# Kernel optimization log

Hardware: AMD Instinct MI355X
Metric: run time of the kernel (lower is better)

## Reference

```python
import jax, jax.numpy as jnp
import numpy as np

B, C_IN, C_OUT, F, K = 4, 64, 64, 50000, 16
BN_EPS = 1e-5


def setup_inputs() -> dict:
    key = jax.random.key(0)
    k1, k2, k3, k4 = jax.random.split(key, 4)
    fea = jax.random.normal(k1, (B, C_IN, F), dtype=jnp.float32)
    ring_n = jax.random.randint(k2, (B, F, K), 0, F, dtype=jnp.int64)
    # Conv1d(kernel_size=1) weight [out, in] and bias [out]
    W = jax.random.normal(k3, (C_OUT, C_IN), dtype=jnp.float32) / np.sqrt(C_IN)
    b = jax.random.normal(k4, (C_OUT,), dtype=jnp.float32) * 0.01
    gamma = jnp.ones((C_OUT,), dtype=jnp.float32)
    beta = jnp.zeros((C_OUT,), dtype=jnp.float32)
    return {"fea": fea, "ring_n": ring_n, "W": W, "b": b, "gamma": gamma, "beta": beta}


def reference(fea, ring_n, W, b, gamma, beta):
    # Note: original torch code overwrites the cat result, so only the
    # NEIGHBOR features are summed (center face excluded).
    def gather_sum(f, r):  # f: [C, F], r: [F, K]
        return f[:, r].sum(axis=-1)  # [C, F, K] -> [C, F]

    summed = jax.vmap(gather_sum)(fea, ring_n)  # [B, C_in, F]
    # 1x1 conv == channel matmul
    y = jnp.einsum("oc,bcf->bof", W, summed) + b[None, :, None]  # [B, C_out, F]
    # BatchNorm1d (training mode): stats over (batch, faces) per channel
    mean = y.mean(axis=(0, 2), keepdims=True)
    var = y.var(axis=(0, 2), keepdims=True)  # biased, as torch BN uses for normalization
    y = (y - mean) * jax.lax.rsqrt(var + BN_EPS)
    y = y * gamma[None, :, None] + beta[None, :, None]
    return jax.nn.relu(y)
```

## Files before the change

kernel.cpp:

```cpp
#include <hip/hip_runtime.h>
#include <hip/hip_bf16.h>
#include <stdint.h>

#define Bn 4
#define Cn 64
#define Fn 50000
#define Kn 16
#define NTOT (Bn*Fn)
#define EPS 1e-5f

typedef unsigned short u16;
typedef unsigned int u32;
typedef __attribute__((ext_vector_type(8))) short short8;
typedef __attribute__((ext_vector_type(4))) float f32x4;
typedef __attribute__((ext_vector_type(4))) int i32x4;
typedef __attribute__((ext_vector_type(4))) unsigned int u32x4;

__device__ __forceinline__ u16 f2bf(float x) {
  __hip_bfloat16 h = __float2bfloat16(x);
  return *reinterpret_cast<u16*>(&h);
}
__device__ __forceinline__ u32 pack2(float a, float b) {
  return (u32)f2bf(a) | ((u32)f2bf(b) << 16);
}

__global__ __launch_bounds__(256) void k1_mfma(
    const float* __restrict__ fea, const float* __restrict__ W,
    u32* __restrict__ Gt) {
  const int b = blockIdx.y;
  const int f0 = blockIdx.x * 128;
  const int t = threadIdx.x;
  const int l = t & 63;
  const int quad = l >> 4;
  const int lane15 = l & 15;
  const int wv = t >> 6;
  __shared__ float a_s[64][129];

  short8 afr[4][2];
  #pragma unroll
  for (int ot = 0; ot < 4; ot++) {
    #pragma unroll
    for (int kk = 0; kk < 2; kk++) {
      const float* wr = W + (ot * 16 + lane15) * 64 + kk * 32 + quad * 8;
      float4 wa = *(const float4*)wr;
      float4 wb = *(const float4*)(wr + 4);
      union { short8 v; u32 u[4]; } fr;
      fr.u[0] = pack2(wa.x, wa.y); fr.u[1] = pack2(wa.z, wa.w);
      fr.u[2] = pack2(wb.x, wb.y); fr.u[3] = pack2(wb.z, wb.w);
      afr[ot][kk] = fr.v;
    }
  }

  {
    const float* fb = fea + (size_t)b * Cn * Fn;
    const int f4 = t & 31;
    const int cbase = t >> 5;
    const bool fvalid = (f0 + f4 * 4) < Fn;
    #pragma unroll
    for (int jj = 0; jj < 8; jj++) {
      int c = cbase + jj * 8;
      float4 v = make_float4(0.f, 0.f, 0.f, 0.f);
      if (fvalid) v = *(const float4*)(fb + (size_t)c * Fn + f0 + f4 * 4);
      *(float4*)&a_s[c][f4 * 4] = v;
    }
  }
  __syncthreads();

  f32x4 acc[4][2];
  #pragma unroll
  for (int ot = 0; ot < 4; ot++)
    #pragma unroll
    for (int ft = 0; ft < 2; ft++) acc[ot][ft] = (f32x4){0.f, 0.f, 0.f, 0.f};

  #pragma unroll
  for (int ft = 0; ft < 2; ft++) {
    const int fl = wv * 32 + ft * 16 + lane15;
    float x[16];
    #pragma unroll
    for (int j = 0; j < 8; j++) x[j] = a_s[quad * 8 + j][fl];
    #pragma unroll
    for (int j = 0; j < 8; j++) x[8 + j] = a_s[32 + quad * 8 + j][fl];
    union { short8 s; u32 u[4]; } b0, b1;
    #pragma unroll
    for (int p = 0; p < 4; p++) {
      b0.u[p] = pack2(x[2 * p], x[2 * p + 1]);
      b1.u[p] = pack2(x[8 + 2 * p], x[8 + 2 * p + 1]);
    }
    #pragma unroll
    for (int ot = 0; ot < 4; ot++) {
      acc[ot][ft] = __builtin_amdgcn_mfma_f32_16x16x32_bf16(afr[ot][0], b0.s, acc[ot][ft], 0, 0, 0);
      acc[ot][ft] = __builtin_amdgcn_mfma_f32_16x16x32_bf16(afr[ot][1], b1.s, acc[ot][ft], 0, 0, 0);
    }
  }

  __syncthreads();
  u32* ts = (u32*)&a_s[0][0];
  #pragma unroll
  for (int ot = 0; ot < 4; ot++) {
    #pragma unroll
    for (int ft = 0; ft < 2; ft++) {
      int fl = wv * 32 + ft * 16 + lane15;
      uint2 pv;
      pv.x = pack2(acc[ot][ft][0], acc[ot][ft][1]);
      pv.y = pack2(acc[ot][ft][2], acc[ot][ft][3]);
      *(uint2*)&ts[fl * 36 + ot * 8 + quad * 2] = pv;
    }
  }
  __syncthreads();
  #pragma unroll
  for (int j = 0; j < 4; j++) {
    int o = j * 1024 + t * 4;
    int fl = o >> 5, sl = o & 31;
    if (f0 + fl < Fn) {
      u32x4 vv = *(const u32x4*)&ts[fl * 36 + sl];
      *(u32x4*)(Gt + ((size_t)b * Fn + f0 + fl) * 32 + sl) = vv;
    }
  }
}

template<int WRITE_BF16>
__global__ __launch_bounds__(256) void k2_gather(
    const u32* __restrict__ Gt, const int* __restrict__ ring,
    const float* __restrict__ bias, u32* __restrict__ Y, float* __restrict__ outF,
    float* __restrict__ gsum, float* __restrict__ gsum2) {
  const int bid = blockIdx.x;
  const int b = (bid & 7) >> 1;
  const int sub = ((bid >> 3) << 1) | (bid & 1);
  const int t = threadIdx.x;
  const int gid = t >> 3;
  const int cs = t & 7;

  __shared__ float rs[32][68];
  __shared__ float rs2[32][68];

  float bv[8];
  #pragma unroll
  for (int i = 0; i < 8; i++) bv[i] = bias[cs * 8 + i];

  const u32* Gb = Gt + (size_t)b * Fn * 32;
  const int* rb = ring + (size_t)b * Fn * Kn;

  float sacc[8], s2acc[8];
  #pragma unroll
  for (int i = 0; i < 8; i++) { sacc[i] = 0.f; s2acc[i] = 0.f; }

  const int ntiles = (Fn + 31) / 32;

  int tile = sub;
  i32x4 r0, r1, r2, r3;
  if (tile < ntiles) {
    int fa = tile * 32 + gid;
    int fc = fa < Fn ? fa : Fn - 1;
    const i32x4* rp = (const i32x4*)(rb + (size_t)fc * Kn);
    r0 = __builtin_nontemporal_load(&rp[0]);
    r1 = __builtin_nontemporal_load(&rp[1]);
    r2 = __builtin_nontemporal_load(&rp[2]);
    r3 = __builtin_nontemporal_load(&rp[3]);
  }

  for (; tile < ntiles; tile += 512) {
    const int fa = tile * 32 + gid;
    const bool valid = fa < Fn;
    int idx[16] = {r0[0],r0[1],r0[2],r0[3], r1[0],r1[1],r1[2],r1[3],
                   r2[0],r2[1],r2[2],r2[3], r3[0],r3[1],r3[2],r3[3]};

    const int ntile = tile + 512;
    if (ntile < ntiles) {
      int nfa = ntile * 32 + gid;
      int nfc = nfa < Fn ? nfa : Fn - 1;
      const i32x4* rp = (const i32x4*)(rb + (size_t)nfc * Kn);
      r0 = __builtin_nontemporal_load(&rp[0]);
      r1 = __builtin_nontemporal_load(&rp[1]);
      r2 = __builtin_nontemporal_load(&rp[2]);
      r3 = __builtin_nontemporal_load(&rp[3]);
    }

    float acc[8];
    #pragma unroll
    for (int i = 0; i < 8; i++) acc[i] = 0.f;

    u32x4 v[8];
    #pragma unroll
    for (int k = 0; k < 8; k++)
      v[k] = *(const u32x4*)(Gb + (size_t)idx[k] * 32 + cs * 4);
    #pragma unroll
    for (int k = 0; k < 8; k++) {
      #pragma unroll
      for (int p = 0; p < 4; p++) {
        u32 uu = v[k][p];
        acc[2*p]   += __uint_as_float(uu << 16);
        acc[2*p+1] += __uint_as_float(uu & 0xffff0000u);
      }
    }
    #pragma unroll
    for (int k = 0; k < 8; k++)
      v[k] = *(const u32x4*)(Gb + (size_t)idx[8 + k] * 32 + cs * 4);
    #pragma unroll
    for (int k = 0; k < 8; k++) {
      #pragma unroll
      for (int p = 0; p < 4; p++) {
        u32 uu = v[k][p];
        acc[2*p]   += __uint_as_float(uu << 16);
        acc[2*p+1] += __uint_as_float(uu & 0xffff0000u);
      }
    }

    float yv[8];
    #pragma unroll
    for (int i = 0; i < 8; i++) yv[i] = acc[i] + bv[i];

    if (valid) {
      if (WRITE_BF16) {
        u32x4 pv;
        pv[0] = pack2(yv[0], yv[1]); pv[1] = pack2(yv[2], yv[3]);
        pv[2] = pack2(yv[4], yv[5]); pv[3] = pack2(yv[6], yv[7]);
        __builtin_nontemporal_store(pv,
            (u32x4*)(Y + ((size_t)b * Fn + fa) * 32 + cs * 4));
      } else {
        #pragma unroll
        for (int i = 0; i < 8; i++)
          outF[((size_t)b * 64 + cs * 8 + i) * Fn + fa] = yv[i];
      }
      #pragma unroll
      for (int i = 0; i < 8; i++) {
        sacc[i] += yv[i];
        s2acc[i] += yv[i] * yv[i];
      }
    }
  }

  #pragma unroll
  for (int i = 0; i < 8; i++) {
    rs[gid][cs * 8 + i] = sacc[i];
    rs2[gid][cs * 8 + i] = s2acc[i];
  }
  __syncthreads();
  if (t < 64) {
    float s = 0.f;
    #pragma unroll
    for (int g = 0; g < 32; g++) s += rs[g][t];
    atomicAdd(&gsum[t], s);
  } else if (t < 128) {
    const int ch = t - 64;
    float s2 = 0.f;
    #pragma unroll
    for (int g = 0; g < 32; g++) s2 += rs2[g][ch];
    atomicAdd(&gsum2[ch], s2);
  }
}

__global__ void k3_stats(const float* __restrict__ gsum, const float* __restrict__ gsum2,
                         const float* __restrict__ gamma, const float* __restrict__ beta,
                         float* __restrict__ ab) {
  int o = threadIdx.x;
  if (o < 64) {
    float inv = 1.0f / (float)NTOT;
    float mean = gsum[o] * inv;
    float var = gsum2[o] * inv - mean * mean;
    float r = rsqrtf(var + EPS);
    float a = gamma[o] * r;
    ab[o] = a;
    ab[64 + o] = beta[o] - mean * a;
  }
}

__global__ __launch_bounds__(256) void k4_norm_bf(
    const u32* __restrict__ Y, const float* __restrict__ gsum,
    const float* __restrict__ gsum2, const float* __restrict__ gamma,
    const float* __restrict__ beta, float* __restrict__ out) {
  const int b = blockIdx.y;
  const int f0 = blockIdx.x * 64;
  const int t = threadIdx.x;
  __shared__ u32 ys[32][65];

  #pragma unroll
  for (int j = 0; j < 2; j++) {
    int o = j * 1024 + t * 4;
    int fl = o >> 5, sl = o & 31;
    u32x4 vv = (u32x4)(0u);
    if (f0 + fl < Fn)
      vv = *(const u32x4*)(Y + ((size_t)b * Fn + f0 + fl) * 32 + sl);
    ys[sl + 0][fl] = vv[0]; ys[sl + 1][fl] = vv[1];
    ys[sl + 2][fl] = vv[2]; ys[sl + 3][fl] = vv[3];
  }
  __syncthreads();

  const float inv = 1.0f / (float)NTOT;
  const int fi = t & 15, g = t >> 4;
  const int fbase = 4 * fi;
  #pragma unroll
  for (int j = 0; j < 4; j++) {
    int ch = g * 4 + j;
    float mean = gsum[ch] * inv;
    float var = gsum2[ch] * inv - mean * mean;
    float a = gamma[ch] * rsqrtf(var + EPS);
    float cc = beta[ch] - mean * a;
    if (f0 + fbase < Fn) {
      const int c2 = ch >> 1;
      const bool hi = ch & 1;
      float r[4];
      #pragma unroll
      for (int rr = 0; rr < 4; rr++) {
        u32 u = ys[c2][fbase + rr];
        float xv = __uint_as_float(hi ? (u & 0xffff0000u) : (u << 16));
        r[rr] = fmaxf(fmaf(xv, a, cc), 0.f);
      }
      float4 res = make_float4(r[0], r[1], r[2], r[3]);
      *(float4*)(out + ((size_t)b * 64 + ch) * Fn + f0 + fbase) = res;
    }
  }
}

__global__ __launch_bounds__(256) void k4_norm_f32(float* __restrict__ out,
                                                   const float* __restrict__ ab) {
  int i = blockIdx.x * 256 + threadIdx.x;
  int o = (i / (Fn / 4)) & 63;
  float a = ab[o], c = ab[64 + o];
  float4 v = ((float4*)out)[i];
  v.x = fmaxf(fmaf(v.x, a, c), 0.f);
  v.y = fmaxf(fmaf(v.y, a, c), 0.f);
  v.z = fmaxf(fmaf(v.z, a, c), 0.f);
  v.w = fmaxf(fmaf(v.w, a, c), 0.f);
  ((float4*)out)[i] = v;
}

extern "C" void kernel_launch(void* const* d_in, const int* in_sizes, int n_in,
                              void* d_out, int out_size, void* d_ws, size_t ws_size,
                              hipStream_t stream) {
  const float* fea   = (const float*)d_in[0];
  const int*   ring  = (const int*)d_in[1];
  const float* W     = (const float*)d_in[2];
  const float* bias  = (const float*)d_in[3];
  const float* gamma = (const float*)d_in[4];
  const float* beta  = (const float*)d_in[5];
  float* out = (float*)d_out;

  u32* Gt = (u32*)d_ws;
  const size_t gtBytes = (size_t)Bn * Fn * 32 * 4;
  const size_t yBytes  = (size_t)Bn * Fn * 32 * 4;
  const bool bf16y = ws_size >= gtBytes + yBytes + 1024;

  u32* Y = Gt + (size_t)Bn * Fn * 32;
  float* gsum  = bf16y ? (float*)((char*)d_ws + gtBytes + yBytes)
                       : (float*)((char*)d_ws + gtBytes);
  float* gsum2 = gsum + 64;
  float* ab    = gsum + 128;

  hipMemsetAsync(gsum, 0, 2 * 64 * sizeof(float), stream);
  k1_mfma<<<dim3((Fn + 127) / 128, Bn), 256, 0, stream>>>(fea, W, Gt);
  if (bf16y) {
    k2_gather<1><<<dim3(2048), 256, 0, stream>>>(Gt, ring, bias, Y, out, gsum, gsum2);
    k4_norm_bf<<<dim3((Fn + 63) / 64, Bn), 256, 0, stream>>>(Y, gsum, gsum2, gamma, beta, out);
  } else {
    k2_gather<0><<<dim3(2048), 256, 0, stream>>>(Gt, ring, bias, Y, out, gsum, gsum2);
    k3_stats<<<1, 64, 0, stream>>>(gsum, gsum2, gamma, beta, ab);
    k4_norm_f32<<<dim3((Bn * Cn * Fn / 4) / 256), 256, 0, stream>>>(out, ab);
  }
}
```

Measured before the change: 202.5 us.

## Fuse gather, stats and normalization into one cooperative persistent kernel

Replaces the separate gather and normalize kernels with a single cooperative kernel. It gathers neighbor sums, accumulates the batch-norm statistics, performs a grid-wide sync, then normalizes the bf16 intermediate through a shared-memory transpose. The memset is folded into the first kernel. This removes a launch and a memset, at the cost of a grid barrier and fewer resident blocks in the gather phase, with a fallback to the old path if the cooperative launch fails.

```diff
diff --git a/kernel.cpp b/kernel.cpp
--- a/kernel.cpp
+++ b/kernel.cpp
@@ -1,6 +1,9 @@
 #include <hip/hip_runtime.h>
 #include <hip/hip_bf16.h>
+#include <hip/hip_cooperative_groups.h>
 #include <stdint.h>
+
+namespace cg = cooperative_groups;
 
 #define Bn 4
 #define Cn 64
@@ -8,11 +11,13 @@
 #define Kn 16
 #define NTOT (Bn*Fn)
 #define EPS 1e-5f
+#define NSUB 2048
 
 typedef unsigned short u16;
 typedef unsigned int u32;
 typedef __attribute__((ext_vector_type(8))) short short8;
 typedef __attribute__((ext_vector_type(4))) float f32x4;
+typedef __attribute__((ext_vector_type(2))) float f32x2;
 typedef __attribute__((ext_vector_type(4))) int i32x4;
 typedef __attribute__((ext_vector_type(4))) unsigned int u32x4;
 
@@ -23,10 +28,16 @@
 __device__ __forceinline__ u32 pack2(float a, float b) {
   return (u32)f2bf(a) | ((u32)f2bf(b) << 16);
 }
+__device__ __forceinline__ f32x2 up2(u32 uu) {
+  f32x2 r;
+  r.x = __uint_as_float(uu << 16);
+  r.y = __uint_as_float(uu & 0xffff0000u);
+  return r;
+}
 
 __global__ __launch_bounds__(256) void k1_mfma(
     const float* __restrict__ fea, const float* __restrict__ W,
-    u32* __restrict__ Gt) {
+    u32* __restrict__ Gt, float* __restrict__ gsum) {
   const int b = blockIdx.y;
   const int f0 = blockIdx.x * 128;
   const int t = threadIdx.x;
@@ -36,6 +47,8 @@
   const int wv = t >> 6;
   __shared__ float a_s[64][129];
 
+  if (blockIdx.x == 0 && b == 0 && t < 128) gsum[t] = 0.f;
+
   short8 afr[4][2];
   #pragma unroll
   for (int ot = 0; ot < 4; ot++) {
@@ -114,6 +127,167 @@
     if (f0 + fl < Fn) {
       u32x4 vv = *(const u32x4*)&ts[fl * 36 + sl];
       *(u32x4*)(Gt + ((size_t)b * Fn + f0 + fl) * 32 + sl) = vv;
+    }
+  }
+}
+
+__global__ __launch_bounds__(256) void k2f(
+    const u32* __restrict__ Gt, const int* __restrict__ ring,
+    const float* __restrict__ bias, u32* __restrict__ Y,
+    float* __restrict__ gsum, const float* __restrict__ gamma,
+    const float* __restrict__ beta, float* __restrict__ out) {
+  const int t = threadIdx.x;
+  const int gid = t >> 3;
+  const int cs = t & 7;
+  const int ntiles = (Fn + 31) / 32;
+
+  __shared__ union SM {
+    struct { float rs[32][68]; float rs2[32][68]; } s;
+    u32 ys[32][34];
+  } sm;
+
+  f32x2 bv2[4];
+  #pragma unroll
+  for (int p = 0; p < 4; p++) {
+    bv2[p].x = bias[cs * 8 + 2 * p];
+    bv2[p].y = bias[cs * 8 + 2 * p + 1];
+  }
+
+  f32x2 sacc2[4], s2acc2[4];
+  #pragma unroll
+  for (int p = 0; p < 4; p++) { sacc2[p] = (f32x2)(0.f); s2acc2[p] = (f32x2)(0.f); }
+
+  for (int vs = blockIdx.x; vs < NSUB; vs += gridDim.x) {
+    const int b = (vs & 7) >> 1;
+    const int sub = ((vs >> 3) << 1) | (vs & 1);
+    const u32* Gb = Gt + (size_t)b * Fn * 32;
+    const int* rb = ring + (size_t)b * Fn * Kn;
+
+    int tile = sub;
+    i32x4 r0, r1, r2, r3;
+    if (tile < ntiles) {
+      int fa = tile * 32 + gid;
+      int fc = fa < Fn ? fa : Fn - 1;
+      const i32x4* rp = (const i32x4*)(rb + (size_t)fc * Kn);
+      r0 = __builtin_nontemporal_load(&rp[0]);
+      r1 = __builtin_nontemporal_load(&rp[1]);
+      r2 = __builtin_nontemporal_load(&rp[2]);
+      r3 = __builtin_nontemporal_load(&rp[3]);
+    }
+
+    for (; tile < ntiles; tile += 512) {
+      const int fa = tile * 32 + gid;
+      const bool valid = fa < Fn;
+      int idx[16] = {r0[0],r0[1],r0[2],r0[3], r1[0],r1[1],r1[2],r1[3],
+                     r2[0],r2[1],r2[2],r2[3], r3[0],r3[1],r3[2],r3[3]};
+
+      const int ntile = tile + 512;
+      if (ntile < ntiles) {
+        int nfa = ntile * 32 + gid;
+        int nfc = nfa < Fn ? nfa : Fn - 1;
+        const i32x4* rp = (const i32x4*)(rb + (size_t)nfc * Kn);
+        r0 = __builtin_nontemporal_load(&rp[0]);
+        r1 = __builtin_nontemporal_load(&rp[1]);
+        r2 = __builtin_nontemporal_load(&rp[2]);
+        r3 = __builtin_nontemporal_load(&rp[3]);
+      }
+
+      f32x2 acc2[4];
+      #pragma unroll
+      for (int p = 0; p < 4; p++) acc2[p] = bv2[p];
+
+      u32x4 v[8];
+      #pragma unroll
+      for (int k = 0; k < 8; k++)
+        v[k] = *(const u32x4*)(Gb + (size_t)idx[k] * 32 + cs * 4);
+      #pragma unroll
+      for (int k = 0; k < 8; k++) {
+        #pragma unroll
+        for (int p = 0; p < 4; p++) acc2[p] += up2(v[k][p]);
+      }
+      #pragma unroll
+      for (int k = 0; k < 8; k++)
+        v[k] = *(const u32x4*)(Gb + (size_t)idx[8 + k] * 32 + cs * 4);
+      #pragma unroll
+      for (int k = 0; k < 8; k++) {
+        #pragma unroll
+        for (int p = 0; p < 4; p++) acc2[p] += up2(v[k][p]);
+      }
+
+      if (valid) {
+        u32x4 pv;
+        pv[0] = pack2(acc2[0].x, acc2[0].y); pv[1] = pack2(acc2[1].x, acc2[1].y);
+        pv[2] = pack2(acc2[2].x, acc2[2].y); pv[3] = pack2(acc2[3].x, acc2[3].y);
+        *(u32x4*)(Y + ((size_t)b * Fn + fa) * 32 + cs * 4) = pv;
+        #pragma unroll
+        for (int p = 0; p < 4; p++) {
+          sacc2[p] += acc2[p];
+          s2acc2[p] += acc2[p] * acc2[p];
+        }
+      }
+    }
+  }
+
+  #pragma unroll
+  for (int p = 0; p < 4; p++) {
+    sm.s.rs[gid][cs * 8 + 2 * p] = sacc2[p].x;
+    sm.s.rs[gid][cs * 8 + 2 * p + 1] = sacc2[p].y;
+    sm.s.rs2[gid][cs * 8 + 2 * p] = s2acc2[p].x;
+    sm.s.rs2[gid][cs * 8 + 2 * p + 1] = s2acc2[p].y;
+  }
+  __syncthreads();
+  if (t < 64) {
+    float s = 0.f;
+    #pragma unroll
+    for (int g = 0; g < 32; g++) s += sm.s.rs[g][t];
+    atomicAdd(&gsum[t], s);
+  } else if (t < 128) {
+    const int ch = t - 64;
+    float s2 = 0.f;
+    #pragma unroll
+    for (int g = 0; g < 32; g++) s2 += sm.s.rs2[g][ch];
+    atomicAdd(&gsum[64 + ch], s2);
+  }
+
+  cg::this_grid().sync();
+
+  const int ch = t >> 2, fg = t & 3;
+  const float inv = 1.0f / (float)NTOT;
+  const float mean = gsum[ch] * inv;
+  const float var = gsum[64 + ch] * inv - mean * mean;
+  const float a_ = gamma[ch] * rsqrtf(var + EPS);
+  const float c_ = beta[ch] - mean * a_;
+  const int c2 = ch >> 1;
+  const bool hi = ch & 1;
+
+  for (int vs = blockIdx.x; vs < NSUB; vs += gridDim.x) {
+    const int b = (vs & 7) >> 1;
+    const int sub = ((vs >> 3) << 1) | (vs & 1);
+    const u32* Yb = Y + (size_t)b * Fn * 32;
+    for (int tile = sub; tile < ntiles; tile += 512) {
+      __syncthreads();
+      {
+        const int fl = t >> 3, sl = (t & 7) * 4;
+        int fa = tile * 32 + fl;
+        u32x4 vv = (u32x4)(0u);
+        if (fa < Fn) vv = *(const u32x4*)(Yb + (size_t)fa * 32 + sl);
+        sm.ys[sl + 0][fl] = vv[0]; sm.ys[sl + 1][fl] = vv[1];
+        sm.ys[sl + 2][fl] = vv[2]; sm.ys[sl + 3][fl] = vv[3];
+      }
+      __syncthreads();
+      const int fbase = tile * 32 + fg * 8;
+      if (fbase < Fn) {
+        float r[8];
+        #pragma unroll
+        for (int j = 0; j < 8; j++) {
+          u32 u = sm.ys[c2][fg * 8 + j];
+          float xv = __uint_as_float(hi ? (u & 0xffff0000u) : (u << 16));
+          r[j] = fmaxf(fmaf(xv, a_, c_), 0.f);
+        }
+        float* ob = out + ((size_t)b * 64 + ch) * Fn + fbase;
+        *(float4*)ob = make_float4(r[0], r[1], r[2], r[3]);
+        *(float4*)(ob + 4) = make_float4(r[4], r[5], r[6], r[7]);
+      }
     }
   }
 }
@@ -346,13 +520,27 @@
   float* gsum2 = gsum + 64;
   float* ab    = gsum + 128;
 
-  hipMemsetAsync(gsum, 0, 2 * 64 * sizeof(float), stream);
-  k1_mfma<<<dim3((Fn + 127) / 128, Bn), 256, 0, stream>>>(fea, W, Gt);
+  k1_mfma<<<dim3((Fn + 127) / 128, Bn), 256, 0, stream>>>(fea, W, Gt, gsum);
+
+  bool done = false;
   if (bf16y) {
-    k2_gather<1><<<dim3(2048), 256, 0, stream>>>(Gt, ring, bias, Y, out, gsum, gsum2);
-    k4_norm_bf<<<dim3((Fn + 63) / 64, Bn), 256, 0, stream>>>(Y, gsum, gsum2, gamma, beta, out);
+    int nb = 0;
+    hipError_t oe = hipOccupancyMaxActiveBlocksPerMultiprocessor(&nb, k2f, 256, 0);
+    if (oe == hipSuccess && nb > 0) {
+      int G = nb * 256;
+      if (G > NSUB) G = NSUB;
+      void* args[] = {(void*)&Gt, (void*)&ring, (void*)&bias, (void*)&Y,
+                      (void*)&gsum, (void*)&gamma, (void*)&beta, (void*)&out};
+      hipError_t le = hipLaunchCooperativeKernel((const void*)k2f, dim3(G),
+                                                 dim3(256), args, 0, stream);
+      done = (le == hipSuccess);
+    }
+    if (!done) {
+      k2_gather<1><<<dim3(NSUB), 256, 0, stream>>>(Gt, ring, bias, Y, out, gsum, gsum2);
+      k4_norm_bf<<<dim3((Fn + 63) / 64, Bn), 256, 0, stream>>>(Y, gsum, gsum2, gamma, beta, out);
+    }
   } else {
-    k2_gather<0><<<dim3(2048), 256, 0, stream>>>(Gt, ring, bias, Y, out, gsum, gsum2);
+    k2_gather<0><<<dim3(NSUB), 256, 0, stream>>>(Gt, ring, bias, Y, out, gsum, gsum2);
     k3_stats<<<1, 64, 0, stream>>>(gsum, gsum2, gamma, beta, ab);
     k4_norm_f32<<<dim3((Bn * Cn * Fn / 4) / 256), 256, 0, stream>>>(out, ab);
   }
```

Measured after the change: 304.5 us. 50.4% more time.
